# Kernel tuning notes

Measured on AMD Instinct MI355X. Metric: run time of the kernel, lower is better.

The kernel has to match this reference:

```python
import jax, jax.numpy as jnp
import numpy as np

B, NC, NS = 128, 32, 128          # graphs, compound atoms/graph, pocket sites/graph
NV, NSITE = B * NC, B * NS        # 4096 compound atoms, 16384 site atoms total
EV, ES = NV * 4, NSITE * 8        # edge counts (avg degree 4 / 8)
FDIM, SDIM = 82, 32               # atom feature dims
H, HS, HP, HI = 128, 128, 128, 64 # hidden_vert, hidden_site, hidden_prot, hidden_int
D, K = 3, 8                       # GNN depth (both), attention heads
P = B * NC * NS                   # 524288 site-atom pairs


def setup_inputs():
    key = jax.random.key(0)
    ks = iter(jax.random.split(key, 80))
    def nrm(shape, s=0.05):
        return jax.random.normal(next(ks), shape, jnp.float32) * s
    inp = {}
    inp['x_vert'] = jax.random.normal(next(ks), (NV, FDIM), jnp.float32)
    inp['vert_src'] = jax.random.randint(next(ks), (EV,), 0, NV)
    inp['vert_dst'] = jax.random.randint(next(ks), (EV,), 0, NV)
    inp['vert_batch'] = jnp.repeat(jnp.arange(B, dtype=jnp.int32), NC)
    inp['W_emb'] = nrm((FDIM, H)); inp['b_emb'] = jnp.zeros((H,), jnp.float32)
    inp['Wa_main'] = nrm((D, K, H, H)); inp['Wa_super'] = nrm((D, K, H, H))
    inp['Wv'] = nrm((D, K, H, H)); inp['Wb'] = nrm((D, K, H))
    inp['Wm2s'] = nrm((D, K * H, H)); inp['Ws2m'] = nrm((D, H, H))
    inp['Wsup'] = nrm((D, H, H)); inp['Wself'] = nrm((D, H, H))
    inp['Wzm1'] = nrm((D, H, H)); inp['Wzm2'] = nrm((D, H, H))
    inp['Wzs1'] = nrm((D, H, H)); inp['Wzs2'] = nrm((D, H, H))
    for tag in ('m', 's'):
        inp['Wih_' + tag] = nrm((H, 3 * H)); inp['Whh_' + tag] = nrm((H, 3 * H))
        inp['bih_' + tag] = jnp.zeros((3 * H,), jnp.float32)
        inp['bhh_' + tag] = jnp.zeros((3 * H,), jnp.float32)
    inp['x_site'] = jax.random.normal(next(ks), (NSITE, SDIM), jnp.float32)
    inp['site_src'] = jax.random.randint(next(ks), (ES,), 0, NSITE)
    inp['site_dst'] = jax.random.randint(next(ks), (ES,), 0, NSITE)
    inp['W0'] = nrm((2 * SDIM, HS)); inp['b0'] = jnp.zeros((HS,), jnp.float32)
    inp['Wconv'] = nrm((D - 1, 2 * HS, HS)); inp['bconv'] = jnp.zeros((D - 1, HS), jnp.float32)
    inp['Wout'] = nrm((SDIM + D * HS, HP)); inp['bout'] = jnp.zeros((HP,), jnp.float32)
    inp['Wis'] = nrm((7, HP, HI)); inp['bis'] = jnp.zeros((7, HI), jnp.float32)
    inp['Wic'] = nrm((7, H, HI)); inp['bic'] = jnp.zeros((7, HI), jnp.float32)
    # block-diagonal all-pairs index (every site x every compound atom within a graph)
    g = jnp.arange(B, dtype=jnp.int32)
    a = jnp.arange(NS, dtype=jnp.int32)
    c = jnp.arange(NC, dtype=jnp.int32)
    inp['idx_site'] = jnp.broadcast_to(g[:, None, None] * NS + a[None, :, None], (B, NS, NC)).reshape(-1)
    inp['idx_comp'] = jnp.broadcast_to(g[:, None, None] * NC + c[None, None, :], (B, NS, NC)).reshape(-1)
    return inp


def _leaky(x):
    return jnp.where(x > 0, x, 0.1 * x)


def _gru(x, h, Wih, Whh, bih, bhh):
    gi = x @ Wih + bih
    gh = h @ Whh + bhh
    ir, iz, inn = jnp.split(gi, 3, axis=-1)
    hr, hz, hn = jnp.split(gh, 3, axis=-1)
    r = jax.nn.sigmoid(ir + hr)
    z = jax.nn.sigmoid(iz + hz)
    n = jnp.tanh(inn + r * hn)
    return (1.0 - z) * n + z * h


def reference(x_vert, vert_src, vert_dst, vert_batch, W_emb, b_emb,
              Wa_main, Wa_super, Wv, Wb, Wm2s, Ws2m, Wsup, Wself,
              Wzm1, Wzm2, Wzs1, Wzs2,
              Wih_m, Whh_m, bih_m, bhh_m, Wih_s, Whh_s, bih_s, bhh_s,
              x_site, site_src, site_dst, W0, b0, Wconv, bconv, Wout, bout,
              Wis, bis, Wic, bic, idx_site, idx_comp):
    seg = jax.ops.segment_sum
    # ---- GraphConv_module: embedding + GWM (graph warp) iterations ----
    vert = _leaky(x_vert @ W_emb + b_emb)                      # [NV, H]
    supe = seg(vert, vert_batch, num_segments=B)               # [B, H] super node init
    for d in range(D):
        # local vertex message passing
        nei = seg(vert[vert_src], vert_dst, num_segments=NV)
        main_self = _leaky((vert + nei) @ Wself[d])
        # multi-head main -> super attention (segment softmax over each graph)
        am = jnp.tanh(jnp.einsum('nd,kde->kne', vert, Wa_main[d]))        # [K,NV,H]
        asup = jnp.tanh(jnp.einsum('bd,kde->kbe', supe, Wa_super[d]))     # [K,B,H]
        score = jnp.einsum('kne,ke->nk', am * asup[:, vert_batch], Wb[d]) # [NV,K]
        smax = jax.ops.segment_max(score, vert_batch, num_segments=B)
        e = jnp.exp(score - smax[vert_batch])
        attn = e / seg(e, vert_batch, num_segments=B)[vert_batch]         # [NV,K]
        msg = jnp.einsum('nd,kde->nke', vert, Wv[d])                      # [NV,K,H]
        m2s = seg(attn[:, :, None] * msg, vert_batch, num_segments=B)     # [B,K,H]
        main_to_super = jnp.tanh(m2s.reshape(B, K * H) @ Wm2s[d])         # [B,H]
        super_to_main = jnp.tanh(supe @ Ws2m[d])[vert_batch]              # [NV,H]
        # warp gates + shared GRU updates
        zm = jax.nn.sigmoid(main_self @ Wzm1[d] + super_to_main @ Wzm2[d])
        vert = _gru((1 - zm) * main_self + zm * super_to_main, vert, Wih_m, Whh_m, bih_m, bhh_m)
        super_self = jnp.tanh(supe @ Wsup[d])
        zs = jax.nn.sigmoid(super_self @ Wzs1[d] + main_to_super @ Wzs2[d])
        supe = _gru((1 - zs) * super_self + zs * main_to_super, supe, Wih_s, Whh_s, bih_s, bhh_s)
    # ---- AtomConv_module on protein sites ----
    h = x_site
    feats = [h]
    for i in range(D):
        nei = seg(h[site_src], site_dst, num_segments=NSITE)
        W = W0 if i == 0 else Wconv[i - 1]
        b = b0 if i == 0 else bconv[i - 1]
        h = _leaky(jnp.concatenate([h, nei], axis=-1) @ W + b)
        feats.append(h)
    site = _leaky(jnp.concatenate(feats, axis=-1) @ Wout + bout)  # [NSITE, HP]
    # ---- Interaction_pred_module: 7-head gather-multiply-reduce over pairs ----
    preds = []
    for i in range(7):
        pa = _leaky(site @ Wis[i] + bis[i])   # [NSITE, HI]
        pg = _leaky(vert @ Wic[i] + bic[i])   # [NV, HI]
        preds.append(jnp.sum(pa[idx_site] * pg[idx_comp], axis=1))  # [P]
    return jnp.stack(preds, axis=1)           # [P, 7]
```

## Files before the change

### kernel.cpp

```cpp
#include <hip/hip_runtime.h>
#include <hip/hip_bf16.h>

typedef unsigned short u16;
typedef unsigned int u32;

static constexpr int cNV = 4096, cEV = 16384, cB = 128, cNC = 32, cNS = 128;
static constexpr int cNSITE = 16384, cES = 131072;
static constexpr int cH = 128, cK8 = 8, cHI = 64;

__device__ __forceinline__ float leakyf(float x){ return x > 0.f ? x : 0.1f * x; }
__device__ __forceinline__ float sigm(float x){ return 1.f / (1.f + __expf(-x)); }

typedef __attribute__((ext_vector_type(4))) short short4v;
typedef __attribute__((ext_vector_type(4))) float f32x4;

__device__ __forceinline__ u16 f2bu(float x){
  __hip_bfloat16 h = __float2bfloat16(x);
  return *(u16*)&h;
}
__device__ __forceinline__ float bf2f(u16 u){
  __hip_bfloat16 h; *(u16*)&h = u;
  return __bfloat162float(h);
}

__global__ void zero_i_k(int* __restrict__ p, int n){
  int i = blockIdx.x * 256 + threadIdx.x;
  if (i < n) p[i] = 0;
}
__global__ void copy_i_k(const int* __restrict__ s, int* __restrict__ d, int n){
  int i = blockIdx.x * 256 + threadIdx.x;
  if (i < n) d[i] = s[i];
}
__global__ void count_k(const int* __restrict__ dst, int* __restrict__ cnt, int ne){
  int i = blockIdx.x * 256 + threadIdx.x;
  if (i < ne) atomicAdd(&cnt[dst[i]], 1);
}
__global__ void scan_k(const int* __restrict__ cnt, int* __restrict__ off, int n){
  __shared__ int part[256];
  int t = threadIdx.x;
  int chunk = n >> 8;
  int base = t * chunk;
  int s = 0;
  for (int j = 0; j < chunk; j++) s += cnt[base + j];
  part[t] = s;
  __syncthreads();
  for (int d = 1; d < 256; d <<= 1) {
    int v = (t >= d) ? part[t - d] : 0;
    __syncthreads();
    part[t] += v;
    __syncthreads();
  }
  int run = (t == 0) ? 0 : part[t - 1];
  for (int j = 0; j < chunk; j++) { off[base + j] = run; run += cnt[base + j]; }
  if (t == 255) off[n] = run;
}
__global__ void fill_k(const int* __restrict__ src, const int* __restrict__ dst,
                       int* __restrict__ cur, int* __restrict__ perm, int ne){
  int i = blockIdx.x * 256 + threadIdx.x;
  if (i < ne) {
    int p = atomicAdd(&cur[dst[i]], 1);
    perm[p] = src[i];
  }
}

__global__ void gather128_f_k(const float* __restrict__ h, const int* __restrict__ off,
                              const int* __restrict__ perm, float* __restrict__ nei){
  int row = blockIdx.x, t = threadIdx.x;
  int b = off[row], e = off[row + 1];
  float s = 0.f;
  for (int i = b; i < e; i++) s += h[(long)perm[i] * 128 + t];
  nei[(long)row * 128 + t] = s;
}
__global__ void gather128_b_k(const u16* __restrict__ h, const int* __restrict__ off,
                              const int* __restrict__ perm, u16* __restrict__ nei){
  int row = blockIdx.x, t = threadIdx.x;
  int b = off[row], e = off[row + 1];
  float s = 0.f;
  for (int i = b; i < e; i++) s += bf2f(h[(long)perm[i] * 128 + t]);
  nei[(long)row * 128 + t] = f2bu(s);
}
__global__ void gather32_k(const float* __restrict__ h, const int* __restrict__ off,
                           const int* __restrict__ perm, u16* __restrict__ nei){
  int t = threadIdx.x;
  int row = blockIdx.x * 8 + (t >> 5), c = t & 31;
  int b = off[row], e = off[row + 1];
  float s = 0.f;
  for (int i = b; i < e; i++) s += h[(long)perm[i] * 32 + c];
  nei[(long)row * 32 + c] = f2bu(s);
}

__global__ void cvtw_k(const float* __restrict__ src, u16* __restrict__ dst,
                       int K, int krsh, int N, int ldw, int cshift, int cs){
  long i = (long)blockIdx.x * 256 + threadIdx.x;
  int Kr = 1 << krsh;
  if (i >= (long)N * Kr) return;
  int n = (int)(i >> krsh), k = (int)(i & (Kr - 1));
  float v = 0.f;
  if (k < K) v = src[(long)k * ldw + (long)(n >> cshift) * cs + (n & ((1 << cshift) - 1))];
  dst[i] = f2bu(v);
}

struct GSegs {
  const u16* Wt[4];
  const float* bias[4];
  const float* addA[4];
  void* C[4];
  u16* C2[4];
  int nb_end[4];
  int N[4];
  int Kr[4];
  int act[4];
  int odt[4];
  int nsegs;
};

__global__ __launch_bounds__(256) void gemm_g(
    const void* __restrict__ A0, const void* __restrict__ A1,
    const void* __restrict__ A2, const void* __restrict__ A3,
    int dt0, int dt1, int dt2, int dt3,
    int k1, int k2, int k3, int K, int M,
    GSegs segs, const float* __restrict__ ep1, const float* __restrict__ ep2)
{
  __shared__ __align__(16) u16 As[64 * 136];
  __shared__ __align__(16) u16 Bs[64 * 136];
  const int t = threadIdx.x;
  const int l = t & 63, w = t >> 6;
  const int wr = w >> 1, wc = w & 1;
  const int lr = l & 15, lh = l >> 4;

  const int nwg = gridDim.x * gridDim.y;
  const int bid = blockIdx.y * gridDim.x + blockIdx.x;
  const int cpx = nwg >> 3;
  const int swz = (bid & 7) * cpx + (bid >> 3);
  const int bx = swz % gridDim.x, by = swz / gridDim.x;

  const u16* Wt = nullptr; const float* bias = nullptr; const float* addA = nullptr;
  void* C = nullptr; u16* C2 = nullptr;
  int Nn = 0, Kr = 0, act = 0, odt = 0, nb0 = 0;
  {
    int nbs = 0;
    #pragma unroll
    for (int s = 0; s < 4; s++) {
      if (s < segs.nsegs) {
        int e = segs.nb_end[s];
        if (bx >= nbs && bx < e) {
          Wt = segs.Wt[s]; bias = segs.bias[s]; addA = segs.addA[s];
          C = segs.C[s]; C2 = segs.C2[s];
          Nn = segs.N[s]; Kr = segs.Kr[s]; act = segs.act[s]; odt = segs.odt[s];
          nb0 = nbs;
        }
        nbs = e;
      }
    }
  }
  const int n0 = (bx - nb0) * 64;
  const int m0 = by * 64;
  const int w1 = k2 - k1, w2 = k3 - k2, w3 = K - k3;

  f32x4 acc[2][2];
  #pragma unroll
  for (int i = 0; i < 2; i++)
    #pragma unroll
    for (int j = 0; j < 2; j++)
      acc[i][j] = (f32x4){0.f, 0.f, 0.f, 0.f};

  const int arow = t >> 2, kq = (t & 3) * 32;
  const int bcol = t & 63, bq = (t >> 6) * 32;
  const int mg = m0 + arow;

  for (int kt = 0; kt < K; kt += 128) {
    #pragma unroll
    for (int sub = 0; sub < 4; sub++) {
      const int kg0 = kt + kq + sub * 8;
      const void* bp; int st, wseg, dt;
      if (kg0 < k1)      { bp = A0; st = 0;  wseg = k1; dt = dt0; }
      else if (kg0 < k2) { bp = A1; st = k1; wseg = w1; dt = dt1; }
      else if (kg0 < k3) { bp = A2; st = k2; wseg = w2; dt = dt2; }
      else               { bp = A3; st = k3; wseg = w3; dt = dt3; }
      uint4 v;
      if (dt == 0 && addA == nullptr && kg0 + 8 <= st + wseg) {
        v = *(const uint4*)((const u16*)bp + (long)mg * wseg + (kg0 - st));
      } else {
        float f[8];
        #pragma unroll
        for (int j = 0; j < 8; j++) {
          int kg = kg0 + j;
          float x = 0.f;
          if (kg < K) {
            long o = (long)mg * wseg + (kg - st);
            x = dt ? ((const float*)bp)[o] : bf2f(((const u16*)bp)[o]);
            if (addA != nullptr) x += addA[(long)mg * K + kg];
          }
          f[j] = x;
        }
        v.x = (u32)f2bu(f[0]) | ((u32)f2bu(f[1]) << 16);
        v.y = (u32)f2bu(f[2]) | ((u32)f2bu(f[3]) << 16);
        v.z = (u32)f2bu(f[4]) | ((u32)f2bu(f[5]) << 16);
        v.w = (u32)f2bu(f[6]) | ((u32)f2bu(f[7]) << 16);
      }
      *(uint4*)&As[arow * 136 + kq + sub * 8] = v;
    }
    #pragma unroll
    for (int sub = 0; sub < 4; sub++) {
      uint4 v = *(const uint4*)(Wt + (long)(n0 + bcol) * Kr + kt + bq + sub * 8);
      *(uint4*)&Bs[bcol * 136 + bq + sub * 8] = v;
    }
    __syncthreads();
    #pragma unroll
    for (int ks = 0; ks < 8; ks++) {
      short4v a0 = *(short4v*)&As[(wr * 32 + 0 * 16 + lr) * 136 + ks * 16 + lh * 4];
      short4v a1 = *(short4v*)&As[(wr * 32 + 1 * 16 + lr) * 136 + ks * 16 + lh * 4];
      short4v b0 = *(short4v*)&Bs[(wc * 32 + 0 * 16 + lr) * 136 + ks * 16 + lh * 4];
      short4v b1 = *(short4v*)&Bs[(wc * 32 + 1 * 16 + lr) * 136 + ks * 16 + lh * 4];
      acc[0][0] = __builtin_amdgcn_mfma_f32_16x16x16bf16_1k(a0, b0, acc[0][0], 0, 0, 0);
      acc[0][1] = __builtin_amdgcn_mfma_f32_16x16x16bf16_1k(a0, b1, acc[0][1], 0, 0, 0);
      acc[1][0] = __builtin_amdgcn_mfma_f32_16x16x16bf16_1k(a1, b0, acc[1][0], 0, 0, 0);
      acc[1][1] = __builtin_amdgcn_mfma_f32_16x16x16bf16_1k(a1, b1, acc[1][1], 0, 0, 0);
    }
    __syncthreads();
  }
  #pragma unroll
  for (int ri = 0; ri < 2; ri++) {
    #pragma unroll
    for (int ci = 0; ci < 2; ci++) {
      int col = n0 + wc * 32 + ci * 16 + lr;
      float bv = (bias != nullptr) ? bias[col] : 0.f;
      #pragma unroll
      for (int e = 0; e < 4; e++) {
        int row = m0 + wr * 32 + ri * 16 + lh * 4 + e;
        float v = acc[ri][ci][e] + bv;
        if (act == 1) v = leakyf(v);
        else if (act == 2) v = tanhf(v);
        else if (act == 3) v = sigm(v);
        else if (act == 4) {
          int b = row >> 5;
          float zm = sigm(v + ep1[b * 128 + col]);
          float msv = bf2f(((const u16*)A0)[(long)row * k1 + col]);
          v = (1.f - zm) * msv + zm * ep2[b * 128 + col];
        }
        long o = (long)row * Nn + col;
        if (odt == 0) ((float*)C)[o] = v;
        else if (odt == 1) ((u16*)C)[o] = f2bu(v);
        else { ((float*)C)[o] = v; C2[o] = f2bu(v); }
      }
    }
  }
}

__global__ void supe_init_k(const float* __restrict__ vert, float* __restrict__ supe){
  int b = blockIdx.x, c = threadIdx.x;
  float s = 0.f;
  for (int i = 0; i < cNC; i++) s += vert[(b * cNC + i) * cH + c];
  supe[b * cH + c] = s;
}

__global__ __launch_bounds__(256) void supe_pre_k(
    const float* __restrict__ supe,
    const float* __restrict__ Wa_super_d, const float* __restrict__ Ws2m_d,
    const float* __restrict__ Wzm2_d, const float* __restrict__ Wsup_d,
    const float* __restrict__ Whh_s, const float* __restrict__ bhh_s,
    float* __restrict__ asup, float* __restrict__ s2m, float* __restrict__ s2mz,
    float* __restrict__ sself, float* __restrict__ gh_s)
{
  __shared__ float srow[cH];
  __shared__ float s2ml[cH];
  int b = blockIdx.x, t = threadIdx.x;
  if (t < cH) srow[t] = supe[b * cH + t];
  __syncthreads();
  for (int j = 0; j < 4; j++) {
    int c = t + j * 256;
    int head = c >> 7, e = c & 127;
    const float* Wp = Wa_super_d + head * 16384 + e;
    float s = 0.f;
    for (int d2 = 0; d2 < cH; d2++) s += srow[d2] * Wp[d2 * 128];
    asup[b * 1024 + c] = tanhf(s);
  }
  if (t < cH) {
    float s = 0.f;
    for (int d2 = 0; d2 < cH; d2++) s += srow[d2] * Ws2m_d[d2 * 128 + t];
    float v = tanhf(s);
    s2ml[t] = v; s2m[b * cH + t] = v;
  } else {
    int c = t - cH;
    float s = 0.f;
    for (int d2 = 0; d2 < cH; d2++) s += srow[d2] * Wsup_d[d2 * 128 + c];
    sself[b * cH + c] = tanhf(s);
  }
  {
    int c = t;
    float s = 0.f;
    for (int d2 = 0; d2 < cH; d2++) s += srow[d2] * Whh_s[d2 * 384 + c];
    gh_s[b * 384 + c] = s + bhh_s[c];
    if (t < cH) {
      int c2 = 256 + t;
      float s2 = 0.f;
      for (int d2 = 0; d2 < cH; d2++) s2 += srow[d2] * Whh_s[d2 * 384 + c2];
      gh_s[b * 384 + c2] = s2 + bhh_s[c2];
    }
  }
  __syncthreads();
  if (t < cH) {
    float s = 0.f;
    for (int d2 = 0; d2 < cH; d2++) s += s2ml[d2] * Wzm2_d[d2 * 128 + t];
    s2mz[b * cH + t] = s;
  }
}

__global__ __launch_bounds__(256) void attn_k(
    const u16* __restrict__ am, const float* __restrict__ asup,
    const float* __restrict__ Wb_d, float* __restrict__ attn)
{
  __shared__ float pw[1024];
  __shared__ float sc[cNC][cK8];
  int b = blockIdx.x, t = threadIdx.x;
  for (int j = 0; j < 4; j++) {
    int c = t + j * 256;
    pw[c] = asup[b * 1024 + c] * Wb_d[c];
  }
  __syncthreads();
  int nl = t >> 3, k = t & 7;
  int n = b * cNC + nl;
  const u16* ar = am + (long)n * 1024 + k * 128;
  const float* pr = pw + k * 128;
  float s = 0.f;
  for (int e = 0; e < 128; e++) s += bf2f(ar[e]) * pr[e];
  sc[nl][k] = s;
  __syncthreads();
  float mx = -1e30f;
  for (int i = 0; i < cNC; i++) mx = fmaxf(mx, sc[i][k]);
  float den = 0.f;
  for (int i = 0; i < cNC; i++) den += __expf(sc[i][k] - mx);
  attn[n * cK8 + k] = __expf(s - mx) / den;
}

__global__ __launch_bounds__(256) void m2s_k(
    const float* __restrict__ attn, const u16* __restrict__ msg,
    const float* __restrict__ Wm2s_d, float* __restrict__ mts)
{
  __shared__ float m2s[1024];
  __shared__ float at[cNC][cK8];
  int b = blockIdx.x, t = threadIdx.x;
  at[t >> 3][t & 7] = attn[(b * cNC + (t >> 3)) * cK8 + (t & 7)];
  __syncthreads();
  for (int j = 0; j < 4; j++) {
    int c = t + j * 256;
    int k = c >> 7;
    float s = 0.f;
    for (int i = 0; i < cNC; i++) s += at[i][k] * bf2f(msg[(long)(b * cNC + i) * 1024 + c]);
    m2s[c] = s;
  }
  __syncthreads();
  if (t < cH) {
    float s = 0.f;
    for (int j = 0; j < 1024; j++) s += m2s[j] * Wm2s_d[j * 128 + t];
    mts[b * cH + t] = tanhf(s);
  }
}

__global__ void ew_gru_k(const u16* __restrict__ gi, const u16* __restrict__ gh,
                         float* __restrict__ h, u16* __restrict__ hb){
  int idx = blockIdx.x * 256 + threadIdx.x;
  if (idx >= cNV * cH) return;
  int n = idx >> 7, c = idx & 127;
  const u16* gir = gi + (long)n * 384;
  const u16* ghr = gh + (long)n * 384;
  float r = sigm(bf2f(gir[c]) + bf2f(ghr[c]));
  float z = sigm(bf2f(gir[128 + c]) + bf2f(ghr[128 + c]));
  float nn = tanhf(bf2f(gir[256 + c]) + r * bf2f(ghr[256 + c]));
  float v = (1.f - z) * nn + z * h[idx];
  h[idx] = v;
  hb[idx] = f2bu(v);
}

__global__ __launch_bounds__(128) void super_upd_k(
    const float* __restrict__ sself, const float* __restrict__ mts,
    const float* __restrict__ gh_s,
    const float* __restrict__ Wzs1_d, const float* __restrict__ Wzs2_d,
    const float* __restrict__ Wih_s, const float* __restrict__ bih_s,
    float* __restrict__ supe)
{
  __shared__ float ss[cH], mt[cH], xs[cH], sr[cH];
  int b = blockIdx.x, t = threadIdx.x;
  ss[t] = sself[b * cH + t];
  mt[t] = mts[b * cH + t];
  sr[t] = supe[b * cH + t];
  __syncthreads();
  float s1 = 0.f, s2 = 0.f;
  for (int d2 = 0; d2 < cH; d2++) {
    s1 += ss[d2] * Wzs1_d[d2 * 128 + t];
    s2 += mt[d2] * Wzs2_d[d2 * 128 + t];
  }
  float zs = sigm(s1 + s2);
  xs[t] = (1.f - zs) * ss[t] + zs * mt[t];
  __syncthreads();
  float g0 = 0.f, g1 = 0.f, g2 = 0.f;
  for (int d2 = 0; d2 < cH; d2++) {
    float x = xs[d2];
    g0 += x * Wih_s[d2 * 384 + t];
    g1 += x * Wih_s[d2 * 384 + 128 + t];
    g2 += x * Wih_s[d2 * 384 + 256 + t];
  }
  g0 += bih_s[t]; g1 += bih_s[128 + t]; g2 += bih_s[256 + t];
  float r = sigm(g0 + gh_s[b * 384 + t]);
  float z = sigm(g1 + gh_s[b * 384 + 128 + t]);
  float nn = tanhf(g2 + r * gh_s[b * 384 + 256 + t]);
  supe[b * cH + t] = (1.f - z) * nn + z * sr[t];
}

__global__ __launch_bounds__(256) void pair_k(
    const u16* __restrict__ pa, const u16* __restrict__ pg, float* __restrict__ out)
{
  __shared__ float pal[cNS][cHI];
  __shared__ float pgl[cNC][cHI + 1];
  int g = blockIdx.x, i = blockIdx.y;
  int t = threadIdx.x;
  for (int l = t; l < cNS * cHI; l += 256) {
    int s = l >> 6, hh = l & 63;
    pal[s][hh] = bf2f(pa[(long)(g * cNS + s) * 448 + i * 64 + hh]);
  }
  for (int l = t; l < cNC * cHI; l += 256) {
    int c = l >> 6, hh = l & 63;
    pgl[c][hh] = bf2f(pg[(long)(g * cNC + c) * 448 + i * 64 + hh]);
  }
  __syncthreads();
  for (int o = t; o < cNS * cNC; o += 256) {
    int s = o >> 5, c = o & 31;
    float sum = 0.f;
    #pragma unroll 8
    for (int hh = 0; hh < cHI; hh++) sum += pal[s][hh] * pgl[c][hh];
    long p = (long)g * (cNS * cNC) + o;
    out[p * 7 + i] = sum;
  }
}

extern "C" void kernel_launch(void* const* d_in, const int* in_sizes, int n_in,
                              void* d_out, int out_size, void* d_ws, size_t ws_size,
                              hipStream_t stream) {
  constexpr long OFF_VERT = 0;
  constexpr long OFF_SUPE = 524288;
  constexpr long OFF_SITE = 1064960;
  constexpr long OFF_ATTN = 3162112;
  constexpr long OFF_ASUP = 3194880;
  constexpr long OFF_S2M = 3325952;
  constexpr long OFF_S2MZ = 3342336;
  constexpr long OFF_SSELF = 3358720;
  constexpr long OFF_GHS = 3375104;
  constexpr long OFF_MTS = 3424256;
  constexpr long OFF_NEI = 3440640;
  constexpr long OFF_TMPA = 3964928;
  constexpr long OFF_MS = 4489216;
  constexpr long OFF_ZMP = 5013504;
  constexpr long OFF_XGRU = 5537792;
  constexpr long OFF_GHM = 6062080;
  constexpr long OFF_GIM = 7634944;
  constexpr long OFF_AM = 9207808;
  constexpr long OFF_MSG = 13402112;
  constexpr long OFF_H1 = 17596416;
  constexpr long OFF_H2 = 19693568;
  constexpr long OFF_H3 = 21790720;
  constexpr long WS_FLOATS = 23887872;
  if (ws_size < (size_t)WS_FLOATS * 4) return;

  constexpr long WT_EMB = 0;
  constexpr long WT_SELF = 16384;
  constexpr long WT_AMAIN = 65536;
  constexpr long WT_V = 458752;
  constexpr long WT_HHM = 851968;
  constexpr long WT_ZM1 = 901120;
  constexpr long WT_IHM = 950272;
  constexpr long WT_W0 = 999424;
  constexpr long WT_CONV = 1015808;
  constexpr long WT_OUT = 1081344;
  constexpr long WT_IS = 1146880;
  constexpr long WT_IC = 1204224;

  const float* x_vert  = (const float*)d_in[0];
  const int*   vsrc    = (const int*)d_in[1];
  const int*   vdst    = (const int*)d_in[2];
  const float* W_emb   = (const float*)d_in[4];
  const float* b_emb   = (const float*)d_in[5];
  const float* Wa_main = (const float*)d_in[6];
  const float* Wa_super= (const float*)d_in[7];
  const float* Wv      = (const float*)d_in[8];
  const float* Wb      = (const float*)d_in[9];
  const float* Wm2s    = (const float*)d_in[10];
  const float* Ws2m    = (const float*)d_in[11];
  const float* Wsup    = (const float*)d_in[12];
  const float* Wself   = (const float*)d_in[13];
  const float* Wzm1    = (const float*)d_in[14];
  const float* Wzm2    = (const float*)d_in[15];
  const float* Wzs1    = (const float*)d_in[16];
  const float* Wzs2    = (const float*)d_in[17];
  const float* Wih_m   = (const float*)d_in[18];
  const float* Whh_m   = (const float*)d_in[19];
  const float* bih_m   = (const float*)d_in[20];
  const float* bhh_m   = (const float*)d_in[21];
  const float* Wih_s   = (const float*)d_in[22];
  const float* Whh_s   = (const float*)d_in[23];
  const float* bih_s   = (const float*)d_in[24];
  const float* bhh_s   = (const float*)d_in[25];
  const float* x_site  = (const float*)d_in[26];
  const int*   ssrc    = (const int*)d_in[27];
  const int*   sdst    = (const int*)d_in[28];
  const float* W0      = (const float*)d_in[29];
  const float* b0      = (const float*)d_in[30];
  const float* Wconv   = (const float*)d_in[31];
  const float* bconv   = (const float*)d_in[32];
  const float* Wout    = (const float*)d_in[33];
  const float* bout    = (const float*)d_in[34];
  const float* Wis     = (const float*)d_in[35];
  const float* bis     = (const float*)d_in[36];
  const float* Wic     = (const float*)d_in[37];
  const float* bic     = (const float*)d_in[38];
  float* out = (float*)d_out;

  float* ws = (float*)d_ws;
  float* vert  = ws + OFF_VERT;
  float* supe  = ws + OFF_SUPE;
  float* attn  = ws + OFF_ATTN;
  float* asup  = ws + OFF_ASUP;
  float* s2m   = ws + OFF_S2M;
  float* s2mz  = ws + OFF_S2MZ;
  float* sself = ws + OFF_SSELF;
  float* gh_s  = ws + OFF_GHS;
  float* mts   = ws + OFF_MTS;
  float* nei   = ws + OFF_NEI;

  u16* vert_b = (u16*)(ws + OFF_ZMP);
  u16* ms_b   = (u16*)(ws + OFF_MS);
  u16* xgru_b = (u16*)(ws + OFF_XGRU);
  u16* ghm_b  = (u16*)(ws + OFF_GHM);
  u16* gim_b  = (u16*)(ws + OFF_GHM + 786432);
  u16* h1b    = (u16*)(ws + OFF_H1);
  u16* h2b    = (u16*)(ws + OFF_H2);
  u16* h3b    = (u16*)(ws + OFF_H3);
  u16* site_b = (u16*)(ws + OFF_SITE);
  u16* am_b   = (u16*)(ws + OFF_AM);
  u16* msg_b  = (u16*)(ws + OFF_MSG);
  u16* nei_sb = (u16*)(ws + OFF_AM);
  u16* pa_b   = (u16*)(ws + OFF_MSG);
  u16* pg_b   = (u16*)(ws + OFF_GIM);
  u16* wbuf   = (u16*)(ws + OFF_H3 + 1048576);

  int* iws   = (int*)(ws + OFF_TMPA);
  int* voff  = iws;
  int* vcur  = iws + 8192;
  int* vperm = iws + 16384;
  int* soff  = iws + 32768;
  int* scur  = iws + 57344;
  int* sperm = iws + 81920;

  auto cvtw = [&](const float* src, long wt_off, int K, int krsh, int N,
                  int ldw, int cshift, int cs){
    long tot = (long)N << krsh;
    cvtw_k<<<dim3((unsigned)((tot + 255) / 256)), 256, 0, stream>>>(
        src, wbuf + wt_off, K, krsh, N, ldw, cshift, cs);
  };
  auto gemm1 = [&](const void* A0, int dt0, const void* A1, int dt1,
                   const void* A2, int dt2, const void* A3, int dt3,
                   int k1, int k2, int k3, int K, int M,
                   long wt_off, int Kr, const float* bias,
                   void* C, u16* C2, int N, int act, int odt,
                   const float* addA = nullptr,
                   const float* ep1 = nullptr, const float* ep2 = nullptr){
    GSegs s{};
    s.Wt[0] = wbuf + wt_off; s.bias[0] = bias; s.addA[0] = addA;
    s.C[0] = C; s.C2[0] = C2;
    s.nb_end[0] = N / 64; s.N[0] = N; s.Kr[0] = Kr; s.act[0] = act; s.odt[0] = odt;
    s.nsegs = 1;
    dim3 g(N / 64, M / 64);
    gemm_g<<<g, 256, 0, stream>>>(A0, A1, A2, A3, dt0, dt1, dt2, dt3,
                                  k1, k2, k3, K, M, s, ep1, ep2);
  };

  zero_i_k<<<16, 256, 0, stream>>>(vcur, cNV);
  count_k<<<cEV / 256, 256, 0, stream>>>(vdst, vcur, cEV);
  scan_k<<<1, 256, 0, stream>>>(vcur, voff, cNV);
  copy_i_k<<<16, 256, 0, stream>>>(voff, vcur, cNV);
  fill_k<<<cEV / 256, 256, 0, stream>>>(vsrc, vdst, vcur, vperm, cEV);
  zero_i_k<<<64, 256, 0, stream>>>(scur, cNSITE);
  count_k<<<cES / 256, 256, 0, stream>>>(sdst, scur, cES);
  scan_k<<<1, 256, 0, stream>>>(scur, soff, cNSITE);
  copy_i_k<<<64, 256, 0, stream>>>(soff, scur, cNSITE);
  fill_k<<<cES / 256, 256, 0, stream>>>(ssrc, sdst, scur, sperm, cES);

  cvtw(W_emb, WT_EMB, 82, 7, 128, 128, 30, 0);
  cvtw(Wself, WT_SELF, 128, 7, 384, 128, 7, 16384);
  cvtw(Wa_main, WT_AMAIN, 128, 7, 3072, 128, 7, 16384);
  cvtw(Wv, WT_V, 128, 7, 3072, 128, 7, 16384);
  cvtw(Whh_m, WT_HHM, 128, 7, 384, 384, 30, 0);
  cvtw(Wzm1, WT_ZM1, 128, 7, 384, 128, 7, 16384);
  cvtw(Wih_m, WT_IHM, 128, 7, 384, 384, 30, 0);
  cvtw(W0, WT_W0, 64, 7, 128, 128, 30, 0);
  cvtw(Wconv, WT_CONV, 256, 8, 256, 128, 7, 32768);
  cvtw(Wout, WT_OUT, 416, 9, 128, 128, 30, 0);
  cvtw(Wis, WT_IS, 128, 7, 448, 64, 6, 8192);
  cvtw(Wic, WT_IC, 128, 7, 448, 64, 6, 8192);

  gemm1(x_vert, 1, x_vert, 1, x_vert, 1, x_vert, 1, 82, 82, 82, 82, cNV,
        WT_EMB, 128, b_emb, vert, vert_b, 128, 1, 2);
  supe_init_k<<<cB, 128, 0, stream>>>(vert, supe);

  for (int d = 0; d < 3; d++) {
    const float* Wa_super_d = Wa_super + (long)d * 131072;
    const float* Wb_d = Wb + (long)d * 1024;
    const float* Wm2s_d = Wm2s + (long)d * 131072;
    const float* Ws2m_d = Ws2m + (long)d * 16384;
    const float* Wsup_d = Wsup + (long)d * 16384;
    const float* Wzm2_d = Wzm2 + (long)d * 16384;
    const float* Wzs1_d = Wzs1 + (long)d * 16384;
    const float* Wzs2_d = Wzs2 + (long)d * 16384;

    gather128_f_k<<<cNV, 128, 0, stream>>>(vert, voff, vperm, nei);

    {
      GSegs s{};
      s.Wt[0] = wbuf + WT_SELF + (long)d * 16384;  s.bias[0] = nullptr;
      s.addA[0] = nei;     s.C[0] = ms_b;  s.C2[0] = nullptr;
      s.N[0] = 128;  s.Kr[0] = 128; s.act[0] = 1; s.odt[0] = 1; s.nb_end[0] = 2;
      s.Wt[1] = wbuf + WT_AMAIN + (long)d * 131072; s.bias[1] = nullptr;
      s.addA[1] = nullptr; s.C[1] = am_b;  s.C2[1] = nullptr;
      s.N[1] = 1024; s.Kr[1] = 128; s.act[1] = 2; s.odt[1] = 1; s.nb_end[1] = 18;
      s.Wt[2] = wbuf + WT_V + (long)d * 131072;     s.bias[2] = nullptr;
      s.addA[2] = nullptr; s.C[2] = msg_b; s.C2[2] = nullptr;
      s.N[2] = 1024; s.Kr[2] = 128; s.act[2] = 0; s.odt[2] = 1; s.nb_end[2] = 34;
      s.Wt[3] = wbuf + WT_HHM;                      s.bias[3] = bhh_m;
      s.addA[3] = nullptr; s.C[3] = ghm_b; s.C2[3] = nullptr;
      s.N[3] = 384;  s.Kr[3] = 128; s.act[3] = 0; s.odt[3] = 1; s.nb_end[3] = 40;
      s.nsegs = 4;
      dim3 g(40, cNV / 64);
      gemm_g<<<g, 256, 0, stream>>>(vert_b, vert_b, vert_b, vert_b, 0, 0, 0, 0,
                                    128, 128, 128, 128, cNV, s, nullptr, nullptr);
    }
    supe_pre_k<<<cB, 256, 0, stream>>>(supe, Wa_super_d, Ws2m_d, Wzm2_d, Wsup_d,
                                       Whh_s, bhh_s, asup, s2m, s2mz, sself, gh_s);
    attn_k<<<cB, 256, 0, stream>>>(am_b, asup, Wb_d, attn);
    m2s_k<<<cB, 256, 0, stream>>>(attn, msg_b, Wm2s_d, mts);
    gemm1(ms_b, 0, ms_b, 0, ms_b, 0, ms_b, 0, 128, 128, 128, 128, cNV,
          WT_ZM1 + (long)d * 16384, 128, nullptr, xgru_b, nullptr, 128, 4, 1,
          nullptr, s2mz, s2m);
    gemm1(xgru_b, 0, xgru_b, 0, xgru_b, 0, xgru_b, 0, 128, 128, 128, 128, cNV,
          WT_IHM, 128, bih_m, gim_b, nullptr, 384, 0, 1);
    ew_gru_k<<<(cNV * cH) / 256, 256, 0, stream>>>(gim_b, ghm_b, vert, vert_b);
    super_upd_k<<<cB, 128, 0, stream>>>(sself, mts, gh_s, Wzs1_d, Wzs2_d,
                                        Wih_s, bih_s, supe);
  }

  gather32_k<<<cNSITE / 8, 256, 0, stream>>>(x_site, soff, sperm, nei_sb);
  gemm1(x_site, 1, nei_sb, 0, nei_sb, 0, nei_sb, 0, 32, 64, 64, 64, cNSITE,
        WT_W0, 128, b0, h1b, nullptr, 128, 1, 1);
  gather128_b_k<<<cNSITE, 128, 0, stream>>>(h1b, soff, sperm, nei_sb);
  gemm1(h1b, 0, nei_sb, 0, nei_sb, 0, nei_sb, 0, 128, 256, 256, 256, cNSITE,
        WT_CONV, 256, bconv, h2b, nullptr, 128, 1, 1);
  gather128_b_k<<<cNSITE, 128, 0, stream>>>(h2b, soff, sperm, nei_sb);
  gemm1(h2b, 0, nei_sb, 0, nei_sb, 0, nei_sb, 0, 128, 256, 256, 256, cNSITE,
        WT_CONV + 32768, 256, bconv + 128, h3b, nullptr, 128, 1, 1);
  gemm1(x_site, 1, h1b, 0, h2b, 0, h3b, 0, 32, 160, 288, 416, cNSITE,
        WT_OUT, 512, bout, site_b, nullptr, 128, 1, 1);

  gemm1(site_b, 0, site_b, 0, site_b, 0, site_b, 0, 128, 128, 128, 128, cNSITE,
        WT_IS, 128, bis, pa_b, nullptr, 448, 1, 1);
  gemm1(vert_b, 0, vert_b, 0, vert_b, 0, vert_b, 0, 128, 128, 128, 128, cNV,
        WT_IC, 128, bic, pg_b, nullptr, 448, 1, 1);
  pair_k<<<dim3(cB, 7), 256, 0, stream>>>(pa_b, pg_b, out);
}
```

Measured before the change: 806.1 us.

## Batch setup kernels, fuse attention with m2s, vectorize bf16 loads

Merges the vertex and site CSR build kernels (zero, count, scan, copy, fill) into paired launches, and replaces twelve weight-conversion launches with one table-driven kernel. Fuses the attention softmax and message-to-super kernels so attention weights stay in shared memory. The Wm2s reduction is split across all 256 threads instead of 128. The attention dot and pair_k staging loads use 16-byte vector reads. The aim is fewer launches and better memory efficiency, at the cost of per-element descriptor selection in the conversion kernel.

```diff
diff --git a/kernel.cpp b/kernel.cpp
--- a/kernel.cpp
+++ b/kernel.cpp
@@ -23,19 +23,20 @@
   return __bfloat162float(h);
 }
 
-__global__ void zero_i_k(int* __restrict__ p, int n){
+__global__ void zero2_i_k(int* __restrict__ a, int na, int* __restrict__ b, int nb){
   int i = blockIdx.x * 256 + threadIdx.x;
-  if (i < n) p[i] = 0;
-}
-__global__ void copy_i_k(const int* __restrict__ s, int* __restrict__ d, int n){
+  if (i < na) a[i] = 0;
+  int j = i - na;
+  if (j >= 0 && j < nb) b[j] = 0;
+}
+__global__ void count2_k(const int* __restrict__ vdst, int* __restrict__ vcnt,
+                         const int* __restrict__ sdst, int* __restrict__ scnt){
   int i = blockIdx.x * 256 + threadIdx.x;
-  if (i < n) d[i] = s[i];
-}
-__global__ void count_k(const int* __restrict__ dst, int* __restrict__ cnt, int ne){
-  int i = blockIdx.x * 256 + threadIdx.x;
-  if (i < ne) atomicAdd(&cnt[dst[i]], 1);
-}
-__global__ void scan_k(const int* __restrict__ cnt, int* __restrict__ off, int n){
+  if (i < cEV) atomicAdd(&vcnt[vdst[i]], 1);
+  int j = i - cEV;
+  if (j >= 0 && j < cES) atomicAdd(&scnt[sdst[j]], 1);
+}
+__device__ void scan_body(const int* __restrict__ cnt, int* __restrict__ off, int n){
   __shared__ int part[256];
   int t = threadIdx.x;
   int chunk = n >> 8;
@@ -54,13 +55,26 @@
   for (int j = 0; j < chunk; j++) { off[base + j] = run; run += cnt[base + j]; }
   if (t == 255) off[n] = run;
 }
-__global__ void fill_k(const int* __restrict__ src, const int* __restrict__ dst,
-                       int* __restrict__ cur, int* __restrict__ perm, int ne){
+__global__ void scan2_k(const int* __restrict__ c1, int* __restrict__ o1, int n1,
+                        const int* __restrict__ c2, int* __restrict__ o2, int n2){
+  if (blockIdx.x == 0) scan_body(c1, o1, n1);
+  else scan_body(c2, o2, n2);
+}
+__global__ void copy2_i_k(const int* __restrict__ s1, int* __restrict__ d1, int n1,
+                          const int* __restrict__ s2, int* __restrict__ d2, int n2){
   int i = blockIdx.x * 256 + threadIdx.x;
-  if (i < ne) {
-    int p = atomicAdd(&cur[dst[i]], 1);
-    perm[p] = src[i];
-  }
+  if (i < n1) d1[i] = s1[i];
+  int j = i - n1;
+  if (j >= 0 && j < n2) d2[j] = s2[j];
+}
+__global__ void fill2_k(const int* __restrict__ vsrc, const int* __restrict__ vdst,
+                        int* __restrict__ vcur, int* __restrict__ vperm,
+                        const int* __restrict__ ssrc, const int* __restrict__ sdst,
+                        int* __restrict__ scur, int* __restrict__ sperm){
+  int i = blockIdx.x * 256 + threadIdx.x;
+  if (i < cEV) { int p = atomicAdd(&vcur[vdst[i]], 1); vperm[p] = vsrc[i]; }
+  int j = i - cEV;
+  if (j >= 0 && j < cES) { int p = atomicAdd(&scur[sdst[j]], 1); sperm[p] = ssrc[j]; }
 }
 
 __global__ void gather128_f_k(const float* __restrict__ h, const int* __restrict__ off,
@@ -89,15 +103,27 @@
   nei[(long)row * 32 + c] = f2bu(s);
 }
 
-__global__ void cvtw_k(const float* __restrict__ src, u16* __restrict__ dst,
-                       int K, int krsh, int N, int ldw, int cshift, int cs){
+struct CvtDesc {
+  const float* src;
+  long start;
+  int K, krsh, ldw, cshift, cs;
+};
+struct CvtTable { CvtDesc d[12]; long total; };
+
+__global__ void cvtw_all_k(CvtTable tab, u16* __restrict__ wbuf){
   long i = (long)blockIdx.x * 256 + threadIdx.x;
-  int Kr = 1 << krsh;
-  if (i >= (long)N * Kr) return;
-  int n = (int)(i >> krsh), k = (int)(i & (Kr - 1));
+  if (i >= tab.total) return;
+  int w = 0;
+  #pragma unroll
+  for (int j = 1; j < 12; j++) if (i >= tab.d[j].start) w = j;
+  const CvtDesc D = tab.d[w];
+  long e = i - D.start;
+  int Kr = 1 << D.krsh;
+  int n = (int)(e >> D.krsh), k = (int)(e & (Kr - 1));
   float v = 0.f;
-  if (k < K) v = src[(long)k * ldw + (long)(n >> cshift) * cs + (n & ((1 << cshift) - 1))];
-  dst[i] = f2bu(v);
+  if (k < D.K)
+    v = D.src[(long)k * D.ldw + (long)(n >> D.cshift) * D.cs + (n & ((1 << D.cshift) - 1))];
+  wbuf[i] = f2bu(v);
 }
 
 struct GSegs {
@@ -306,12 +332,15 @@
   }
 }
 
-__global__ __launch_bounds__(256) void attn_k(
-    const u16* __restrict__ am, const float* __restrict__ asup,
-    const float* __restrict__ Wb_d, float* __restrict__ attn)
+__global__ __launch_bounds__(256) void attn_m2s_k(
+    const u16* __restrict__ am, const u16* __restrict__ msg,
+    const float* __restrict__ asup, const float* __restrict__ Wb_d,
+    const float* __restrict__ Wm2s_d, float* __restrict__ mts)
 {
   __shared__ float pw[1024];
-  __shared__ float sc[cNC][cK8];
+  __shared__ float at[cNC][cK8];
+  __shared__ float m2s[1024];
+  __shared__ float part[256];
   int b = blockIdx.x, t = threadIdx.x;
   for (int j = 0; j < 4; j++) {
     int c = t + j * 256;
@@ -321,39 +350,41 @@
   int nl = t >> 3, k = t & 7;
   int n = b * cNC + nl;
   const u16* ar = am + (long)n * 1024 + k * 128;
-  const float* pr = pw + k * 128;
   float s = 0.f;
-  for (int e = 0; e < 128; e++) s += bf2f(ar[e]) * pr[e];
-  sc[nl][k] = s;
+  for (int j = 0; j < 16; j++) {
+    uint4 v = *(const uint4*)(ar + j * 8);
+    const float* pr = pw + k * 128 + j * 8;
+    s += bf2f(v.x & 0xffff) * pr[0] + bf2f(v.x >> 16) * pr[1]
+       + bf2f(v.y & 0xffff) * pr[2] + bf2f(v.y >> 16) * pr[3]
+       + bf2f(v.z & 0xffff) * pr[4] + bf2f(v.z >> 16) * pr[5]
+       + bf2f(v.w & 0xffff) * pr[6] + bf2f(v.w >> 16) * pr[7];
+  }
+  at[nl][k] = s;
   __syncthreads();
   float mx = -1e30f;
-  for (int i = 0; i < cNC; i++) mx = fmaxf(mx, sc[i][k]);
+  for (int i = 0; i < cNC; i++) mx = fmaxf(mx, at[i][k]);
   float den = 0.f;
-  for (int i = 0; i < cNC; i++) den += __expf(sc[i][k] - mx);
-  attn[n * cK8 + k] = __expf(s - mx) / den;
-}
-
-__global__ __launch_bounds__(256) void m2s_k(
-    const float* __restrict__ attn, const u16* __restrict__ msg,
-    const float* __restrict__ Wm2s_d, float* __restrict__ mts)
-{
-  __shared__ float m2s[1024];
-  __shared__ float at[cNC][cK8];
-  int b = blockIdx.x, t = threadIdx.x;
-  at[t >> 3][t & 7] = attn[(b * cNC + (t >> 3)) * cK8 + (t & 7)];
+  for (int i = 0; i < cNC; i++) den += __expf(at[i][k] - mx);
+  float wgt = __expf(s - mx) / den;
+  __syncthreads();
+  at[nl][k] = wgt;
   __syncthreads();
   for (int j = 0; j < 4; j++) {
     int c = t + j * 256;
-    int k = c >> 7;
-    float s = 0.f;
-    for (int i = 0; i < cNC; i++) s += at[i][k] * bf2f(msg[(long)(b * cNC + i) * 1024 + c]);
-    m2s[c] = s;
-  }
-  __syncthreads();
-  if (t < cH) {
-    float s = 0.f;
-    for (int j = 0; j < 1024; j++) s += m2s[j] * Wm2s_d[j * 128 + t];
-    mts[b * cH + t] = tanhf(s);
+    int k2 = c >> 7;
+    float s2 = 0.f;
+    for (int i = 0; i < cNC; i++) s2 += at[i][k2] * bf2f(msg[(long)(b * cNC + i) * 1024 + c]);
+    m2s[c] = s2;
+  }
+  __syncthreads();
+  {
+    int col = t & 127, half = t >> 7;
+    float s3 = 0.f;
+    for (int j = half * 512; j < half * 512 + 512; j++)
+      s3 += m2s[j] * Wm2s_d[(long)j * 128 + col];
+    part[t] = s3;
+    __syncthreads();
+    if (t < 128) mts[b * 128 + t] = tanhf(part[t] + part[t + 128]);
   }
 }
 
@@ -414,13 +445,23 @@
   __shared__ float pgl[cNC][cHI + 1];
   int g = blockIdx.x, i = blockIdx.y;
   int t = threadIdx.x;
-  for (int l = t; l < cNS * cHI; l += 256) {
-    int s = l >> 6, hh = l & 63;
-    pal[s][hh] = bf2f(pa[(long)(g * cNS + s) * 448 + i * 64 + hh]);
-  }
-  for (int l = t; l < cNC * cHI; l += 256) {
-    int c = l >> 6, hh = l & 63;
-    pgl[c][hh] = bf2f(pg[(long)(g * cNC + c) * 448 + i * 64 + hh]);
+  for (int l = t; l < cNS * 8; l += 256) {
+    int s8 = l >> 3, ch = l & 7;
+    uint4 v = *(const uint4*)(pa + (long)(g * cNS + s8) * 448 + i * 64 + ch * 8);
+    float* dp = &pal[s8][ch * 8];
+    dp[0] = bf2f(v.x & 0xffff); dp[1] = bf2f(v.x >> 16);
+    dp[2] = bf2f(v.y & 0xffff); dp[3] = bf2f(v.y >> 16);
+    dp[4] = bf2f(v.z & 0xffff); dp[5] = bf2f(v.z >> 16);
+    dp[6] = bf2f(v.w & 0xffff); dp[7] = bf2f(v.w >> 16);
+  }
+  {
+    int c = t >> 3, ch = t & 7;
+    uint4 v = *(const uint4*)(pg + (long)(g * cNC + c) * 448 + i * 64 + ch * 8);
+    float* dp = &pgl[c][ch * 8];
+    dp[0] = bf2f(v.x & 0xffff); dp[1] = bf2f(v.x >> 16);
+    dp[2] = bf2f(v.y & 0xffff); dp[3] = bf2f(v.y >> 16);
+    dp[4] = bf2f(v.z & 0xffff); dp[5] = bf2f(v.z >> 16);
+    dp[6] = bf2f(v.w & 0xffff); dp[7] = bf2f(v.w >> 16);
   }
   __syncthreads();
   for (int o = t; o < cNS * cNC; o += 256) {
@@ -439,7 +480,6 @@
   constexpr long OFF_VERT = 0;
   constexpr long OFF_SUPE = 524288;
   constexpr long OFF_SITE = 1064960;
-  constexpr long OFF_ATTN = 3162112;
   constexpr long OFF_ASUP = 3194880;
   constexpr long OFF_S2M = 3325952;
   constexpr long OFF_S2MZ = 3342336;
@@ -473,6 +513,7 @@
   constexpr long WT_OUT = 1081344;
   constexpr long WT_IS = 1146880;
   constexpr long WT_IC = 1204224;
+  constexpr long WT_TOTAL = 1261568;
 
   const float* x_vert  = (const float*)d_in[0];
   const int*   vsrc    = (const int*)d_in[1];
@@ -517,7 +558,6 @@
   float* ws = (float*)d_ws;
   float* vert  = ws + OFF_VERT;
   float* supe  = ws + OFF_SUPE;
-  float* attn  = ws + OFF_ATTN;
   float* asup  = ws + OFF_ASUP;
   float* s2m   = ws + OFF_S2M;
   float* s2mz  = ws + OFF_S2MZ;
@@ -550,12 +590,6 @@
   int* scur  = iws + 57344;
   int* sperm = iws + 81920;
 
-  auto cvtw = [&](const float* src, long wt_off, int K, int krsh, int N,
-                  int ldw, int cshift, int cs){
-    long tot = (long)N << krsh;
-    cvtw_k<<<dim3((unsigned)((tot + 255) / 256)), 256, 0, stream>>>(
-        src, wbuf + wt_off, K, krsh, N, ldw, cshift, cs);
-  };
   auto gemm1 = [&](const void* A0, int dt0, const void* A1, int dt1,
                    const void* A2, int dt2, const void* A3, int dt3,
                    int k1, int k2, int k3, int K, int M,
@@ -573,29 +607,34 @@
                                   k1, k2, k3, K, M, s, ep1, ep2);
   };
 
-  zero_i_k<<<16, 256, 0, stream>>>(vcur, cNV);
-  count_k<<<cEV / 256, 256, 0, stream>>>(vdst, vcur, cEV);
-  scan_k<<<1, 256, 0, stream>>>(vcur, voff, cNV);
-  copy_i_k<<<16, 256, 0, stream>>>(voff, vcur, cNV);
-  fill_k<<<cEV / 256, 256, 0, stream>>>(vsrc, vdst, vcur, vperm, cEV);
-  zero_i_k<<<64, 256, 0, stream>>>(scur, cNSITE);
-  count_k<<<cES / 256, 256, 0, stream>>>(sdst, scur, cES);
-  scan_k<<<1, 256, 0, stream>>>(scur, soff, cNSITE);
-  copy_i_k<<<64, 256, 0, stream>>>(soff, scur, cNSITE);
-  fill_k<<<cES / 256, 256, 0, stream>>>(ssrc, sdst, scur, sperm, cES);
-
-  cvtw(W_emb, WT_EMB, 82, 7, 128, 128, 30, 0);
-  cvtw(Wself, WT_SELF, 128, 7, 384, 128, 7, 16384);
-  cvtw(Wa_main, WT_AMAIN, 128, 7, 3072, 128, 7, 16384);
-  cvtw(Wv, WT_V, 128, 7, 3072, 128, 7, 16384);
-  cvtw(Whh_m, WT_HHM, 128, 7, 384, 384, 30, 0);
-  cvtw(Wzm1, WT_ZM1, 128, 7, 384, 128, 7, 16384);
-  cvtw(Wih_m, WT_IHM, 128, 7, 384, 384, 30, 0);
-  cvtw(W0, WT_W0, 64, 7, 128, 128, 30, 0);
-  cvtw(Wconv, WT_CONV, 256, 8, 256, 128, 7, 32768);
-  cvtw(Wout, WT_OUT, 416, 9, 128, 128, 30, 0);
-  cvtw(Wis, WT_IS, 128, 7, 448, 64, 6, 8192);
-  cvtw(Wic, WT_IC, 128, 7, 448, 64, 6, 8192);
+  zero2_i_k<<<(cNV + cNSITE + 255) / 256, 256, 0, stream>>>(vcur, cNV, scur, cNSITE);
+  count2_k<<<(cEV + cES) / 256, 256, 0, stream>>>(vdst, vcur, sdst, scur);
+  scan2_k<<<2, 256, 0, stream>>>(vcur, voff, cNV, scur, soff, cNSITE);
+  copy2_i_k<<<(cNV + cNSITE + 255) / 256, 256, 0, stream>>>(voff, vcur, cNV, soff, scur, cNSITE);
+  fill2_k<<<(cEV + cES) / 256, 256, 0, stream>>>(vsrc, vdst, vcur, vperm,
+                                                 ssrc, sdst, scur, sperm);
+
+  {
+    CvtTable tab{};
+    auto set = [&](int i, const float* src, long start, int K, int krsh,
+                   int ldw, int cshift, int cs){
+      tab.d[i] = CvtDesc{src, start, K, krsh, ldw, cshift, cs};
+    };
+    set(0,  W_emb,  WT_EMB,  82,  7, 128, 30, 0);
+    set(1,  Wself,  WT_SELF, 128, 7, 128, 7, 16384);
+    set(2,  Wa_main,WT_AMAIN,128, 7, 128, 7, 16384);
+    set(3,  Wv,     WT_V,    128, 7, 128, 7, 16384);
+    set(4,  Whh_m,  WT_HHM,  128, 7, 384, 30, 0);
+    set(5,  Wzm1,   WT_ZM1,  128, 7, 128, 7, 16384);
+    set(6,  Wih_m,  WT_IHM,  128, 7, 384, 30, 0);
+    set(7,  W0,     WT_W0,   64,  7, 128, 30, 0);
+    set(8,  Wconv,  WT_CONV, 256, 8, 128, 7, 32768);
+    set(9,  Wout,   WT_OUT,  416, 9, 128, 30, 0);
+    set(10, Wis,    WT_IS,   128, 7, 64,  6, 8192);
+    set(11, Wic,    WT_IC,   128, 7, 64,  6, 8192);
+    tab.total = WT_TOTAL;
+    cvtw_all_k<<<(unsigned)((WT_TOTAL + 255) / 256), 256, 0, stream>>>(tab, wbuf);
+  }
 
   gemm1(x_vert, 1, x_vert, 1, x_vert, 1, x_vert, 1, 82, 82, 82, 82, cNV,
         WT_EMB, 128, b_emb, vert, vert_b, 128, 1, 2);
@@ -634,8 +673,7 @@
     }
     supe_pre_k<<<cB, 256, 0, stream>>>(supe, Wa_super_d, Ws2m_d, Wzm2_d, Wsup_d,
                                        Whh_s, bhh_s, asup, s2m, s2mz, sself, gh_s);
-    attn_k<<<cB, 256, 0, stream>>>(am_b, asup, Wb_d, attn);
-    m2s_k<<<cB, 256, 0, stream>>>(attn, msg_b, Wm2s_d, mts);
+    attn_m2s_k<<<cB, 256, 0, stream>>>(am_b, msg_b, asup, Wb_d, Wm2s_d, mts);
     gemm1(ms_b, 0, ms_b, 0, ms_b, 0, ms_b, 0, 128, 128, 128, 128, cNV,
           WT_ZM1 + (long)d * 16384, 128, nullptr, xgru_b, nullptr, 128, 4, 1,
           nullptr, s2mz, s2m);
```

After: 1.097 ms. 1.36x slower.
